# Optimization experiments

Hardware: AMD Instinct MI355X
Metric: run time of the kernel (lower is better)

The kernel has to match this reference:

```python
import jax, jax.numpy as jnp
import numpy as np

NEG_NUM = -10000.0


def setup_inputs() -> dict:
    key = jax.random.key(0)
    ks = jax.random.split(key, 7)
    B, L, M, H, A = 32, 2048, 512, 512, 256
    memory = jax.random.normal(ks[0], (B, L, M), dtype=jnp.float32)
    hidden = jax.random.normal(ks[1], (B, H), dtype=jnp.float32)
    mask = jax.random.randint(ks[2], (B, L), 0, 2, dtype=jnp.int32)
    # ensure no fully-masked row (softmax well-defined)
    mask = mask.at[:, 0].set(1)
    # nn.Linear params: W1 (A, M+H), b1 (A,), W2 (1, A), b2 (1,)
    lim1 = 1.0 / np.sqrt(M + H)
    W1 = jax.random.uniform(ks[3], (A, M + H), jnp.float32, -lim1, lim1)
    b1 = jax.random.uniform(ks[4], (A,), jnp.float32, -lim1, lim1)
    lim2 = 1.0 / np.sqrt(A)
    W2 = jax.random.uniform(ks[5], (1, A), jnp.float32, -lim2, lim2)
    b2 = jax.random.uniform(ks[6], (1,), jnp.float32, -lim2, lim2)
    return {"memory": memory, "hidden": hidden, "mask": mask,
            "W1": W1, "b1": b1, "W2": W2, "b2": b2}


def reference(memory, hidden, mask, W1, b1, W2, b2):
    # memory: (B, L, M), hidden: (B, H)
    M = memory.shape[-1]
    # Split W1 so we never materialize the concat: equivalent to
    # Linear(cat([memory, hidden_expanded])) since cat@W1^T = mem@W1m^T + hid@W1h^T
    W1m, W1h = W1[:, :M], W1[:, M:]
    proj = (jnp.einsum('blm,am->bla', memory, W1m)
            + jnp.einsum('bh,ah->ba', hidden, W1h)[:, None, :]
            + b1)                                   # (B, L, A)
    score = jnp.einsum('bla,a->bl', jnp.tanh(proj), W2[0]) + b2[0]  # (B, L)
    score = jnp.where(mask == 0, NEG_NUM, score)
    p_memory = jax.nn.softmax(score, axis=-1)        # (B, L)
    expected_memory = jnp.einsum('bl,blm->bm', p_memory, memory)  # (B, M)
    return expected_memory, p_memory
```

## Files before the change

### kernel.cpp

```cpp
#include <hip/hip_runtime.h>
#include <hip/hip_bf16.h>

constexpr int Bb = 32;
constexpr int Ll = 2048;
constexpr int Mm = 512;
constexpr int Hh = 512;
constexpr int Aa = 256;

typedef __attribute__((ext_vector_type(4))) float f32x4;
typedef __attribute__((ext_vector_type(8))) short short8;
typedef __attribute__((ext_vector_type(4))) unsigned short ushort4v;

__device__ __forceinline__ unsigned short f2bf(float f) {
    __hip_bfloat16 h = __float2bfloat16(f);
    return *reinterpret_cast<unsigned short*>(&h);
}

__device__ __forceinline__ ushort4v cvt4(f32x4 v) {
    ushort4v o;
    o[0] = f2bf(v[0]); o[1] = f2bf(v[1]); o[2] = f2bf(v[2]); o[3] = f2bf(v[3]);
    return o;
}

__device__ __forceinline__ void gload_lds16(const void* g, void* l) {
    __builtin_amdgcn_global_load_lds(
        (const __attribute__((address_space(1))) unsigned int*)g,
        (__attribute__((address_space(3))) unsigned int*)l, 16, 0, 0);
}

__global__ void k_convert_w1m(const float* __restrict__ W1,
                              unsigned short* __restrict__ W1mb) {
    int i = blockIdx.x * 256 + threadIdx.x;
    int a  = i >> 7;
    int mq = (i & 127) << 2;
    f32x4 v = *reinterpret_cast<const f32x4*>(W1 + (size_t)a * (Mm + Hh) + mq);
    int ks = mq >> 5;
    int kb = mq & 31;
    *reinterpret_cast<ushort4v*>(W1mb + (size_t)ks * (Aa * 32) + a * 32 + kb) = cvt4(v);
}

__global__ void k_hb(const float* __restrict__ hidden, const float* __restrict__ W1,
                     const float* __restrict__ b1, float* __restrict__ hb) {
    int b  = blockIdx.x >> 2;
    int hc = blockIdx.x & 3;
    int a  = threadIdx.x;
    __shared__ float sh[128];
    if (threadIdx.x < 128) sh[threadIdx.x] = hidden[b * Hh + hc * 128 + threadIdx.x];
    __syncthreads();
    const float* wrow = W1 + (size_t)a * (Mm + Hh) + Mm + hc * 128;
    float acc = (hc == 0) ? b1[a] : 0.f;
    #pragma unroll 8
    for (int h = 0; h < 128; h += 4) {
        f32x4 w = *reinterpret_cast<const f32x4*>(wrow + h);
        acc += w[0] * sh[h] + w[1] * sh[h + 1] + w[2] * sh[h + 2] + w[3] * sh[h + 3];
    }
    atomicAdd(&hb[b * Aa + a], acc);
}

__launch_bounds__(256, 4)
__global__ void k_score(const float* __restrict__ mem,
                        const unsigned short* __restrict__ W1mb,
                        const float* __restrict__ hb, const float* __restrict__ W2,
                        float* __restrict__ score) {
    __shared__ unsigned short ldsA[2][64 * 32];
    __shared__ unsigned short ldsB[2][256 * 32];

    const int tid  = threadIdx.x;
    const int wave = tid >> 6;
    const int lane = tid & 63;
    const int g = lane >> 4;
    const int r = lane & 15;
    const int blockRow = blockIdx.x * 64;
    const int b = blockRow >> 11;

    f32x4 acc[16];
    #pragma unroll
    for (int ct = 0; ct < 16; ct++) acc[ct] = (f32x4){0.f, 0.f, 0.f, 0.f};

    const int c0 = tid, c1 = tid + 256;
    const float* gA0 = mem + (size_t)(blockRow + (c0 >> 3)) * Mm + (c0 & 7) * 4;
    const float* gA1 = mem + (size_t)(blockRow + (c1 >> 3)) * Mm + (c1 & 7) * 4;
    const char* gB = (const char*)W1mb;

    {
        #pragma unroll
        for (int j = 0; j < 4; ++j)
            gload_lds16(gB + (size_t)(wave * 4 + j) * 1024 + lane * 16,
                        &ldsB[0][(wave * 4 + j) * 512]);
        f32x4 a0 = *reinterpret_cast<const f32x4*>(gA0);
        f32x4 a1 = *reinterpret_cast<const f32x4*>(gA1);
        *reinterpret_cast<ushort4v*>(&ldsA[0][c0 * 4]) = cvt4(a0);
        *reinterpret_cast<ushort4v*>(&ldsA[0][c1 * 4]) = cvt4(a1);
    }
    __syncthreads();

    for (int ks = 0; ks < 16; ++ks) {
        const int cur = ks & 1, nxt = cur ^ 1;
        f32x4 a0, a1;
        if (ks < 15) {
            const int ko = (ks + 1) * 32;
            #pragma unroll
            for (int j = 0; j < 4; ++j)
                gload_lds16(gB + (size_t)(ks + 1) * 16384 + (wave * 4 + j) * 1024 + lane * 16,
                            &ldsB[nxt][(wave * 4 + j) * 512]);
            a0 = *reinterpret_cast<const f32x4*>(gA0 + ko);
            a1 = *reinterpret_cast<const f32x4*>(gA1 + ko);
        }
        short8 af = *reinterpret_cast<const short8*>(&ldsA[cur][(wave * 16 + r) * 32 + g * 8]);
        #pragma unroll
        for (int h = 0; h < 4; ++h) {
            short8 bf[4];
            #pragma unroll
            for (int j = 0; j < 4; ++j)
                bf[j] = *reinterpret_cast<const short8*>(&ldsB[cur][((h * 4 + j) * 16 + r) * 32 + g * 8]);
            #pragma unroll
            for (int j = 0; j < 4; ++j)
                acc[h * 4 + j] = __builtin_amdgcn_mfma_f32_16x16x32_bf16(af, bf[j], acc[h * 4 + j], 0, 0, 0);
        }
        if (ks < 15) {
            *reinterpret_cast<ushort4v*>(&ldsA[nxt][c0 * 4]) = cvt4(a0);
            *reinterpret_cast<ushort4v*>(&ldsA[nxt][c1 * 4]) = cvt4(a1);
        }
        __syncthreads();
    }

    float s[4] = {0.f, 0.f, 0.f, 0.f};
    #pragma unroll
    for (int ct = 0; ct < 16; ++ct) {
        int a = ct * 16 + r;
        float hba = hb[b * Aa + a];
        float w2a = W2[a];
        #pragma unroll
        for (int reg = 0; reg < 4; ++reg) {
            float pr = acc[ct][reg] + hba;
            float e = __expf(2.f * pr);
            float t = (e - 1.f) * __builtin_amdgcn_rcpf(e + 1.f);
            s[reg] += t * w2a;
        }
    }
    #pragma unroll
    for (int off = 1; off < 16; off <<= 1) {
        #pragma unroll
        for (int reg = 0; reg < 4; ++reg) s[reg] += __shfl_xor(s[reg], off, 64);
    }
    if (r == 0) {
        #pragma unroll
        for (int reg = 0; reg < 4; ++reg)
            score[blockRow + wave * 16 + g * 4 + reg] = s[reg];
    }
}

__global__ void k_softmax(const float* __restrict__ score, const int* __restrict__ mask,
                          float* __restrict__ p) {
    __shared__ float smx[4];
    __shared__ float ssm[4];
    int b = blockIdx.x, tid = threadIdx.x;
    float v[8]; int mk[8];
    #pragma unroll
    for (int i = 0; i < 8; i++) {
        int l = i * 256 + tid;
        v[i]  = score[b * Ll + l];
        mk[i] = mask[b * Ll + l];
    }
    float mx = -1e30f;
    #pragma unroll
    for (int i = 0; i < 8; i++) if (mk[i]) mx = fmaxf(mx, v[i]);
    for (int off = 1; off < 64; off <<= 1) mx = fmaxf(mx, __shfl_xor(mx, off, 64));
    if ((tid & 63) == 0) smx[tid >> 6] = mx;
    __syncthreads();
    mx = fmaxf(fmaxf(smx[0], smx[1]), fmaxf(smx[2], smx[3]));

    float e[8]; float s = 0.f;
    #pragma unroll
    for (int i = 0; i < 8; i++) { e[i] = mk[i] ? __expf(v[i] - mx) : 0.f; s += e[i]; }
    for (int off = 1; off < 64; off <<= 1) s += __shfl_xor(s, off, 64);
    if ((tid & 63) == 0) ssm[tid >> 6] = s;
    __syncthreads();
    s = ssm[0] + ssm[1] + ssm[2] + ssm[3];
    float inv = 1.f / s;
    #pragma unroll
    for (int i = 0; i < 8; i++) p[b * Ll + i * 256 + tid] = e[i] * inv;
}

__global__ void k_expected(const float* __restrict__ mem, const float* __restrict__ p,
                           float* __restrict__ out) {
    __shared__ f32x4 sred[32][8];
    int b  = blockIdx.x >> 4;
    int mc = blockIdx.x & 15;
    int mi = threadIdx.x & 7;
    int ls = threadIdx.x >> 3;
    const float* base = mem + (size_t)b * Ll * Mm + mc * 32 + mi * 4;
    const float* pb = p + b * Ll;
    f32x4 acc = (f32x4){0.f, 0.f, 0.f, 0.f};
    for (int il = ls; il < Ll; il += 32) {
        float pv = pb[il];
        f32x4 mv = *reinterpret_cast<const f32x4*>(base + (size_t)il * Mm);
        acc += mv * pv;
    }
    sred[ls][mi] = acc;
    __syncthreads();
    #pragma unroll
    for (int s = 16; s > 0; s >>= 1) {
        if (ls < s) sred[ls][mi] += sred[ls + s][mi];
        __syncthreads();
    }
    if (ls == 0)
        *reinterpret_cast<f32x4*>(out + b * Mm + mc * 32 + mi * 4) = sred[0][mi];
}

extern "C" void kernel_launch(void* const* d_in, const int* in_sizes, int n_in,
                              void* d_out, int out_size, void* d_ws, size_t ws_size,
                              hipStream_t stream) {
    const float* memory = (const float*)d_in[0];
    const float* hidden = (const float*)d_in[1];
    const int*   mask   = (const int*)d_in[2];
    const float* W1     = (const float*)d_in[3];
    const float* b1     = (const float*)d_in[4];
    const float* W2     = (const float*)d_in[5];
    float* out = (float*)d_out;

    unsigned short* W1mb = (unsigned short*)d_ws;
    float* hb    = (float*)((char*)d_ws + 256 * 1024);
    float* score = (float*)((char*)d_ws + 256 * 1024 + 32 * 1024);
    float* p = out + Bb * Mm;

    hipMemsetAsync(hb, 0, (size_t)Bb * Aa * sizeof(float), stream);

    k_convert_w1m<<<128, 256, 0, stream>>>(W1, W1mb);
    k_hb<<<128, 256, 0, stream>>>(hidden, W1, b1, hb);
    k_score<<<1024, 256, 0, stream>>>(memory, W1mb, hb, W2, score);
    k_softmax<<<32, 256, 0, stream>>>(score, mask, p);
    k_expected<<<512, 256, 0, stream>>>(memory, p, out);
}
```

Before: 244.2 us.

## Fuse softmax into split-L expected-memory kernel and merge prep kernels

Merges the W1 conversion and hidden-bias kernels into one launch and drops the memset and atomics. Replaces the softmax and expected-memory kernels with a 2048-block kernel where each block recomputes the row softmax stats, writes its 32 probabilities, and produces a partial weighted sum, followed by a small reduction kernel. The score GEMM now prefetches the A tile two steps ahead so global loads overlap more of the MFMA work. The cost is redundant softmax reductions per block (each re-reads 2048 scores and mask values) plus an extra partial buffer round trip.

Measured after the change: 256.6 us. 1.05x slower.

```diff
diff --git a/kernel.cpp b/kernel.cpp
--- a/kernel.cpp
+++ b/kernel.cpp
@@ -28,33 +28,34 @@
         (__attribute__((address_space(3))) unsigned int*)l, 16, 0, 0);
 }
 
-__global__ void k_convert_w1m(const float* __restrict__ W1,
-                              unsigned short* __restrict__ W1mb) {
-    int i = blockIdx.x * 256 + threadIdx.x;
-    int a  = i >> 7;
-    int mq = (i & 127) << 2;
-    f32x4 v = *reinterpret_cast<const f32x4*>(W1 + (size_t)a * (Mm + Hh) + mq);
-    int ks = mq >> 5;
-    int kb = mq & 31;
-    *reinterpret_cast<ushort4v*>(W1mb + (size_t)ks * (Aa * 32) + a * 32 + kb) = cvt4(v);
-}
-
-__global__ void k_hb(const float* __restrict__ hidden, const float* __restrict__ W1,
-                     const float* __restrict__ b1, float* __restrict__ hb) {
-    int b  = blockIdx.x >> 2;
-    int hc = blockIdx.x & 3;
-    int a  = threadIdx.x;
-    __shared__ float sh[128];
-    if (threadIdx.x < 128) sh[threadIdx.x] = hidden[b * Hh + hc * 128 + threadIdx.x];
-    __syncthreads();
-    const float* wrow = W1 + (size_t)a * (Mm + Hh) + Mm + hc * 128;
-    float acc = (hc == 0) ? b1[a] : 0.f;
-    #pragma unroll 8
-    for (int h = 0; h < 128; h += 4) {
-        f32x4 w = *reinterpret_cast<const f32x4*>(wrow + h);
-        acc += w[0] * sh[h] + w[1] * sh[h + 1] + w[2] * sh[h + 2] + w[3] * sh[h + 3];
-    }
-    atomicAdd(&hb[b * Aa + a], acc);
+__global__ void k_prep(const float* __restrict__ W1, const float* __restrict__ hidden,
+                       const float* __restrict__ b1,
+                       unsigned short* __restrict__ W1mb, float* __restrict__ hb) {
+    const int tid = threadIdx.x;
+    if (blockIdx.x < 128) {
+        int i = blockIdx.x * 256 + tid;
+        int a  = i >> 7;
+        int mq = (i & 127) << 2;
+        f32x4 v = *reinterpret_cast<const f32x4*>(W1 + (size_t)a * (Mm + Hh) + mq);
+        int ks = mq >> 5;
+        int kb = mq & 31;
+        *reinterpret_cast<ushort4v*>(W1mb + (size_t)ks * (Aa * 32) + a * 32 + kb) = cvt4(v);
+    } else {
+        int b = blockIdx.x - 128;
+        __shared__ float sh[Hh];
+        sh[tid]       = hidden[b * Hh + tid];
+        sh[tid + 256] = hidden[b * Hh + 256 + tid];
+        __syncthreads();
+        int a = tid;
+        const float* wrow = W1 + (size_t)a * (Mm + Hh) + Mm;
+        float acc = b1[a];
+        #pragma unroll 8
+        for (int h = 0; h < Hh; h += 4) {
+            f32x4 w = *reinterpret_cast<const f32x4*>(wrow + h);
+            acc += w[0] * sh[h] + w[1] * sh[h + 1] + w[2] * sh[h + 2] + w[3] * sh[h + 3];
+        }
+        hb[b * Aa + a] = acc;
+    }
 }
 
 __launch_bounds__(256, 4)
@@ -92,19 +93,23 @@
         *reinterpret_cast<ushort4v*>(&ldsA[0][c0 * 4]) = cvt4(a0);
         *reinterpret_cast<ushort4v*>(&ldsA[0][c1 * 4]) = cvt4(a1);
     }
+    f32x4 p0 = *reinterpret_cast<const f32x4*>(gA0 + 32);
+    f32x4 p1 = *reinterpret_cast<const f32x4*>(gA1 + 32);
     __syncthreads();
 
     for (int ks = 0; ks < 16; ++ks) {
         const int cur = ks & 1, nxt = cur ^ 1;
-        f32x4 a0, a1;
         if (ks < 15) {
-            const int ko = (ks + 1) * 32;
             #pragma unroll
             for (int j = 0; j < 4; ++j)
                 gload_lds16(gB + (size_t)(ks + 1) * 16384 + (wave * 4 + j) * 1024 + lane * 16,
                             &ldsB[nxt][(wave * 4 + j) * 512]);
-            a0 = *reinterpret_cast<const f32x4*>(gA0 + ko);
-            a1 = *reinterpret_cast<const f32x4*>(gA1 + ko);
+            *reinterpret_cast<ushort4v*>(&ldsA[nxt][c0 * 4]) = cvt4(p0);
+            *reinterpret_cast<ushort4v*>(&ldsA[nxt][c1 * 4]) = cvt4(p1);
+        }
+        if (ks < 14) {
+            p0 = *reinterpret_cast<const f32x4*>(gA0 + (ks + 2) * 32);
+            p1 = *reinterpret_cast<const f32x4*>(gA1 + (ks + 2) * 32);
         }
         short8 af = *reinterpret_cast<const short8*>(&ldsA[cur][(wave * 16 + r) * 32 + g * 8]);
         #pragma unroll
@@ -117,10 +122,6 @@
             for (int j = 0; j < 4; ++j)
                 acc[h * 4 + j] = __builtin_amdgcn_mfma_f32_16x16x32_bf16(af, bf[j], acc[h * 4 + j], 0, 0, 0);
         }
-        if (ks < 15) {
-            *reinterpret_cast<ushort4v*>(&ldsA[nxt][c0 * 4]) = cvt4(a0);
-            *reinterpret_cast<ushort4v*>(&ldsA[nxt][c1 * 4]) = cvt4(a1);
-        }
         __syncthreads();
     }
 
@@ -150,62 +151,78 @@
     }
 }
 
-__global__ void k_softmax(const float* __restrict__ score, const int* __restrict__ mask,
-                          float* __restrict__ p) {
-    __shared__ float smx[4];
-    __shared__ float ssm[4];
-    int b = blockIdx.x, tid = threadIdx.x;
+__launch_bounds__(256)
+__global__ void k_exp1(const float* __restrict__ mem, const float* __restrict__ score,
+                       const int* __restrict__ mask,
+                       float* __restrict__ p, float* __restrict__ partial) {
+    const int b   = blockIdx.x >> 6;
+    const int lc  = blockIdx.x & 63;
+    const int tid = threadIdx.x;
+    const int wave = tid >> 6;
+    __shared__ float redmx[4];
+    __shared__ float redsm[4];
+    __shared__ float sp[32];
+    __shared__ f32x4 sacc[128];
+
+    const float* sb = score + b * Ll;
+    const int*   mb = mask + b * Ll;
+
     float v[8]; int mk[8];
     #pragma unroll
     for (int i = 0; i < 8; i++) {
         int l = i * 256 + tid;
-        v[i]  = score[b * Ll + l];
-        mk[i] = mask[b * Ll + l];
+        v[i]  = sb[l];
+        mk[i] = mb[l];
     }
     float mx = -1e30f;
     #pragma unroll
     for (int i = 0; i < 8; i++) if (mk[i]) mx = fmaxf(mx, v[i]);
+    #pragma unroll
     for (int off = 1; off < 64; off <<= 1) mx = fmaxf(mx, __shfl_xor(mx, off, 64));
-    if ((tid & 63) == 0) smx[tid >> 6] = mx;
-    __syncthreads();
-    mx = fmaxf(fmaxf(smx[0], smx[1]), fmaxf(smx[2], smx[3]));
-
-    float e[8]; float s = 0.f;
-    #pragma unroll
-    for (int i = 0; i < 8; i++) { e[i] = mk[i] ? __expf(v[i] - mx) : 0.f; s += e[i]; }
+    if ((tid & 63) == 0) redmx[wave] = mx;
+    __syncthreads();
+    mx = fmaxf(fmaxf(redmx[0], redmx[1]), fmaxf(redmx[2], redmx[3]));
+
+    float s = 0.f;
+    #pragma unroll
+    for (int i = 0; i < 8; i++) s += mk[i] ? __expf(v[i] - mx) : 0.f;
+    #pragma unroll
     for (int off = 1; off < 64; off <<= 1) s += __shfl_xor(s, off, 64);
-    if ((tid & 63) == 0) ssm[tid >> 6] = s;
-    __syncthreads();
-    s = ssm[0] + ssm[1] + ssm[2] + ssm[3];
-    float inv = 1.f / s;
-    #pragma unroll
-    for (int i = 0; i < 8; i++) p[b * Ll + i * 256 + tid] = e[i] * inv;
-}
-
-__global__ void k_expected(const float* __restrict__ mem, const float* __restrict__ p,
-                           float* __restrict__ out) {
-    __shared__ f32x4 sred[32][8];
-    int b  = blockIdx.x >> 4;
-    int mc = blockIdx.x & 15;
-    int mi = threadIdx.x & 7;
-    int ls = threadIdx.x >> 3;
-    const float* base = mem + (size_t)b * Ll * Mm + mc * 32 + mi * 4;
-    const float* pb = p + b * Ll;
+    if ((tid & 63) == 0) redsm[wave] = s;
+    __syncthreads();
+    s = redsm[0] + redsm[1] + redsm[2] + redsm[3];
+    const float inv = 1.f / s;
+
+    if (tid < 32) {
+        int l = lc * 32 + tid;
+        float pv = mb[l] ? __expf(sb[l] - mx) * inv : 0.f;
+        sp[tid] = pv;
+        p[b * Ll + l] = pv;
+    }
+    __syncthreads();
+
+    const int half = tid >> 7, cq = tid & 127;
+    const float* base = mem + ((size_t)b * Ll + lc * 32) * Mm + cq * 4;
     f32x4 acc = (f32x4){0.f, 0.f, 0.f, 0.f};
-    for (int il = ls; il < Ll; il += 32) {
-        float pv = pb[il];
-        f32x4 mv = *reinterpret_cast<const f32x4*>(base + (size_t)il * Mm);
-        acc += mv * pv;
-    }
-    sred[ls][mi] = acc;
-    __syncthreads();
-    #pragma unroll
-    for (int s = 16; s > 0; s >>= 1) {
-        if (ls < s) sred[ls][mi] += sred[ls + s][mi];
-        __syncthreads();
-    }
-    if (ls == 0)
-        *reinterpret_cast<f32x4*>(out + b * Mm + mc * 32 + mi * 4) = sred[0][mi];
+    for (int rr = half; rr < 32; rr += 2)
+        acc += sp[rr] * *reinterpret_cast<const f32x4*>(base + (size_t)rr * Mm);
+    if (half == 1) sacc[cq] = acc;
+    __syncthreads();
+    if (half == 0) {
+        acc += sacc[cq];
+        *reinterpret_cast<f32x4*>(partial + (size_t)blockIdx.x * Mm + cq * 4) = acc;
+    }
+}
+
+__global__ void k_exp2(const float* __restrict__ partial, float* __restrict__ out) {
+    const int b  = blockIdx.x;
+    const int mi = threadIdx.x;
+    const float* pb = partial + (size_t)b * 64 * Mm + mi * 4;
+    f32x4 acc = (f32x4){0.f, 0.f, 0.f, 0.f};
+    #pragma unroll 8
+    for (int c = 0; c < 64; ++c)
+        acc += *reinterpret_cast<const f32x4*>(pb + (size_t)c * Mm);
+    *reinterpret_cast<f32x4*>(out + b * Mm + mi * 4) = acc;
 }
 
 extern "C" void kernel_launch(void* const* d_in, const int* in_sizes, int n_in,
@@ -220,15 +237,13 @@
     float* out = (float*)d_out;
 
     unsigned short* W1mb = (unsigned short*)d_ws;
-    float* hb    = (float*)((char*)d_ws + 256 * 1024);
-    float* score = (float*)((char*)d_ws + 256 * 1024 + 32 * 1024);
+    float* hb      = (float*)((char*)d_ws + 256 * 1024);
+    float* score   = (float*)((char*)d_ws + 288 * 1024);
+    float* partial = (float*)((char*)d_ws + 1024 * 1024);
     float* p = out + Bb * Mm;
 
-    hipMemsetAsync(hb, 0, (size_t)Bb * Aa * sizeof(float), stream);
-
-    k_convert_w1m<<<128, 256, 0, stream>>>(W1, W1mb);
-    k_hb<<<128, 256, 0, stream>>>(hidden, W1, b1, hb);
+    k_prep<<<160, 256, 0, stream>>>(W1, hidden, b1, W1mb, hb);
     k_score<<<1024, 256, 0, stream>>>(memory, W1mb, hb, W2, score);
-    k_softmax<<<32, 256, 0, stream>>>(score, mask, p);
-    k_expected<<<512, 256, 0, stream>>>(memory, p, out);
-}
+    k_exp1<<<2048, 256, 0, stream>>>(memory, score, mask, p, partial);
+    k_exp2<<<32, 128, 0, stream>>>(partial, out);
+}
```
